# Optimization experiments

Hardware: AMD Instinct MI355X
Metric: run time of the kernel (lower is better)

Reference implementation:

```python
import jax, jax.numpy as jnp
import numpy as np

DIM = 4096
HIDDEN = 4096
B, N, M = 2, 512, 2048


def setup_inputs() -> dict:
    key = jax.random.key(0)
    k1, k2, k3, k4 = jax.random.split(key, 4)
    memory = jax.random.normal(k1, (B, M, DIM), dtype=jnp.bfloat16)
    inputs = jax.random.normal(k2, (B, N, DIM), dtype=jnp.bfloat16)
    # Linear(dim, hidden, bias=False): weight is [hidden, dim]; y = x @ W^T
    scale = 1.0 / np.sqrt(DIM)
    wq = (jax.random.normal(k3, (HIDDEN, DIM), dtype=jnp.float32) * scale).astype(jnp.bfloat16)
    wk = (jax.random.normal(k4, (HIDDEN, DIM), dtype=jnp.float32) * scale).astype(jnp.bfloat16)
    return {"memory": memory, "inputs": inputs, "wq": wq, "wk": wk, "seg_num": 100}


def reference(memory, inputs, wq, wk, seg_num):
    # xq = inputs @ Wq^T  [B, N, H];  mk = memory @ Wk^T  [B, M, H]
    xq = jnp.einsum('bnd,hd->bnh', inputs, wq)
    mk = jnp.einsum('bmd,hd->bmh', memory, wk)
    scores = jnp.einsum('bnh,bmh->bnm', xq, mk) / np.sqrt(HIDDEN)  # [B, N, M]
    scores = jax.nn.softmax(scores.astype(jnp.float32), axis=-1).astype(xq.dtype)
    # hist = seg_num - argmax over memory axis, flattened  [B*N]
    hist = (seg_num - jnp.argmax(scores, axis=2)).reshape(-1)
    browse = hist[0] < 4
    output = jnp.einsum('bnm,bmd->bnd', scores, memory)  # [B, N, dim]
    return output, hist, browse
```

## Files before the change

kernel.cpp:

```cpp
#include <hip/hip_runtime.h>

typedef unsigned short u16;
typedef unsigned int   u32;
typedef unsigned long long u64;
typedef __attribute__((ext_vector_type(8))) short bf16x8;
typedef __attribute__((ext_vector_type(8))) unsigned short u16x8;
typedef __attribute__((ext_vector_type(4))) float f32x4;

__device__ __forceinline__ float bf2f(u16 h){ u32 u = ((u32)h)<<16; return __builtin_bit_cast(float, u); }
__device__ __forceinline__ u16 f2bf(float f){
    u32 u = __builtin_bit_cast(u32, f);
    return (u16)((u + 0x7FFFu + ((u>>16)&1u)) >> 16);
}
__device__ __forceinline__ u16 ftrunc_bf(float f){
    return (u16)(__builtin_bit_cast(u32, f) >> 16);
}

__device__ __forceinline__ void gload16(const void* g, void* l){
    __builtin_amdgcn_global_load_lds((const __attribute__((address_space(1))) void*)g,
                                     (__attribute__((address_space(3))) void*)l, 16, 0, 0);
}


__global__ __launch_bounds__(256) void cvt_f2b(
    const float* __restrict__ in, u16* __restrict__ out, long n8)
{
    for (long i = (long)blockIdx.x * 256 + threadIdx.x; i < n8; i += (long)gridDim.x * 256){
        f32x4 a = *(const f32x4*)(in + i*8);
        f32x4 b = *(const f32x4*)(in + i*8 + 4);
        u16x8 o;
        #pragma unroll
        for (int j = 0; j < 4; j++){ o[j] = ftrunc_bf(a[j]); o[j+4] = ftrunc_bf(b[j]); }
        *(u16x8*)(out + i*8) = o;
    }
}

template<int OF32>
__device__ __forceinline__ void gemm_body(
    const u16* __restrict__ A, const u16* __restrict__ B, void* __restrict__ Cv,
    int K, int ldc, int rowA0, int rowB0, float scale,
    u16* lA, u16* lB)
{
    const int t = threadIdx.x, lane = t & 63, w = t >> 6;
    const int wr = w >> 1, wc = w & 1;

    f32x4 acc[4][4];
    #pragma unroll
    for (int i = 0; i < 4; i++)
        #pragma unroll
        for (int j = 0; j < 4; j++) acc[i][j] = (f32x4){0.f,0.f,0.f,0.f};

    const int r0 = t >> 2,         c0 = (t & 3) << 3;
    const int r1 = (t + 256) >> 2, c1 = ((t + 256) & 3) << 3;
    const int laneRow = lane & 15, laneK = (lane >> 4) << 3;

    const int nK = K >> 5;
    for (int kt = 0; kt < nK; ++kt){
        const int kk = kt << 5;
        gload16(A + (size_t)(rowA0 + r0) * K + kk + c0, &lA[t * 8]);
        gload16(B + (size_t)(rowB0 + r0) * K + kk + c0, &lB[t * 8]);
        gload16(A + (size_t)(rowA0 + r1) * K + kk + c1, &lA[(t + 256) * 8]);
        gload16(B + (size_t)(rowB0 + r1) * K + kk + c1, &lB[(t + 256) * 8]);
        __syncthreads();

        bf16x8 af[4], bfv[4];
        #pragma unroll
        for (int mi = 0; mi < 4; mi++)
            af[mi] = *(const bf16x8*)&lA[(wr*64 + mi*16 + laneRow) * 32 + laneK];
        #pragma unroll
        for (int ni = 0; ni < 4; ni++)
            bfv[ni] = *(const bf16x8*)&lB[(wc*64 + ni*16 + laneRow) * 32 + laneK];

        #pragma unroll
        for (int mi = 0; mi < 4; mi++)
            #pragma unroll
            for (int ni = 0; ni < 4; ni++)
                acc[mi][ni] = __builtin_amdgcn_mfma_f32_16x16x32_bf16(af[mi], bfv[ni], acc[mi][ni], 0, 0, 0);
        __syncthreads();
    }

    const int rowBase = rowA0 + wr*64;
    const int colBase = rowB0 + wc*64;
    #pragma unroll
    for (int mi = 0; mi < 4; mi++){
        #pragma unroll
        for (int ni = 0; ni < 4; ni++){
            f32x4 a = acc[mi][ni];
            const int cc = colBase + ni*16 + laneRow;
            const int rr = rowBase + mi*16 + ((lane >> 4) << 2);
            #pragma unroll
            for (int r = 0; r < 4; r++){
                const size_t idx = (size_t)(rr + r) * ldc + cc;
                float v = a[r] * scale;
                if (OF32) ((float*)Cv)[idx] = v;
                else      ((u16*)Cv)[idx]  = f2bf(v);
            }
        }
    }
}

template<int OF32>
__global__ __launch_bounds__(256) void gemm_b16(
    const u16* __restrict__ A, const u16* __restrict__ B, void* __restrict__ Cv,
    int K, int ldc, long aBatch, long bBatch, long cBatch, float scale)
{
    __shared__ u16 lA[128*32];
    __shared__ u16 lB[128*32];
    const int b = blockIdx.z;
    const u16* Ab = A + (size_t)b * aBatch;
    const u16* Bb = B + (size_t)b * bBatch;
    void* Cb = OF32 ? (void*)((float*)Cv + (size_t)b * cBatch)
                    : (void*)((u16*)Cv  + (size_t)b * cBatch);
    gemm_body<OF32>(Ab, Bb, Cb, K, ldc, blockIdx.y * 128, blockIdx.x * 128, scale, lA, lB);
}

__global__ __launch_bounds__(256) void proj_fused(
    const u16* __restrict__ mem16, const u16* __restrict__ wk16, u16* __restrict__ mk16,
    const u16* __restrict__ in16,  const u16* __restrict__ wq16, u16* __restrict__ xq16)
{
    __shared__ u16 lA[128*32];
    __shared__ u16 lB[128*32];
    const int z = blockIdx.z;
    const u16 *A, *B; u16* C;
    if (z < 2){
        A = mem16 + (size_t)z * 2048 * 4096; B = wk16; C = mk16 + (size_t)z * 2048 * 4096;
    } else {
        if (blockIdx.y >= 8) return;
        A = in16; B = wq16; C = xq16;
    }
    gemm_body<0>(A, B, C, 4096, 4096, blockIdx.y * 128, blockIdx.x * 128, 1.0f, lA, lB);
}

__global__ __launch_bounds__(256) void transpose_u16(
    const u16* __restrict__ in, u16* __restrict__ out)
{
    __shared__ u16 tile[64][65];
    const size_t bi = (size_t)blockIdx.z * 2048 * 4096;
    const size_t bo = (size_t)blockIdx.z * 4096 * 2048;
    const int c0 = blockIdx.x * 64;
    const int r0 = blockIdx.y * 64;
    const int x = threadIdx.x & 63, y = threadIdx.x >> 6;
    #pragma unroll
    for (int i = 0; i < 16; i++){
        int r = y + i*4;
        tile[r][x] = in[bi + (size_t)(r0 + r) * 4096 + c0 + x];
    }
    __syncthreads();
    #pragma unroll
    for (int i = 0; i < 16; i++){
        int c = y + i*4;
        out[bo + (size_t)(c0 + c) * 2048 + r0 + x] = tile[x][c];
    }
}

__device__ __forceinline__ u32 shfl_u32(u32 v, int srcx){ return (u32)__shfl_xor((int)v, srcx, 64); }
__device__ __forceinline__ u64 shflxor64(u64 x, int off){
    u32 lo = (u32)x, hi = (u32)(x >> 32);
    lo = shfl_u32(lo, off); hi = shfl_u32(hi, off);
    return (((u64)hi) << 32) | lo;
}

__global__ __launch_bounds__(256) void softmax_argmax16(
    const u16* __restrict__ sc16, u16* __restrict__ probs,
    float* __restrict__ dout, const int* __restrict__ segp)
{
    const int row = blockIdx.x;
    const u16* s = sc16 + (size_t)row * 2048;
    u16* p = probs + (size_t)row * 2048;
    const int t = threadIdx.x, lane = t & 63, w = t >> 6;

    u16x8 rv = *(const u16x8*)(s + (size_t)t * 8);
    float v[8];
    #pragma unroll
    for (int j = 0; j < 8; j++) v[j] = bf2f(rv[j]);

    float mx = v[0];
    #pragma unroll
    for (int j = 1; j < 8; j++) mx = fmaxf(mx, v[j]);
    #pragma unroll
    for (int off = 32; off; off >>= 1) mx = fmaxf(mx, __shfl_xor(mx, off, 64));
    __shared__ float smax[4];
    if (lane == 0) smax[w] = mx;
    __syncthreads();
    mx = fmaxf(fmaxf(smax[0], smax[1]), fmaxf(smax[2], smax[3]));

    float e[8]; float sum = 0.f;
    #pragma unroll
    for (int j = 0; j < 8; j++){ e[j] = expf(v[j] - mx); sum += e[j]; }
    #pragma unroll
    for (int off = 32; off; off >>= 1) sum += __shfl_xor(sum, off, 64);
    __shared__ float ssum[4];
    if (lane == 0) ssum[w] = sum;
    __syncthreads();
    sum = ssum[0] + ssum[1] + ssum[2] + ssum[3];

    u16x8 pv;
    u64 best = 0ull;
    #pragma unroll
    for (int j = 0; j < 8; j++){
        u16 pb = f2bf(e[j] / sum);
        pv[j] = pb;
        u64 key = (((u64)pb) << 32) | (u32)(0x7FFFFFFF - (t*8 + j));
        if (key > best) best = key;
    }
    *(u16x8*)(p + (size_t)t * 8) = pv;

    #pragma unroll
    for (int off = 32; off; off >>= 1){
        u64 o = shflxor64(best, off);
        if (o > best) best = o;
    }
    __shared__ u64 sb[4];
    if (lane == 0) sb[w] = best;
    __syncthreads();
    if (t == 0){
        u64 bb = sb[0];
        if (sb[1] > bb) bb = sb[1];
        if (sb[2] > bb) bb = sb[2];
        if (sb[3] > bb) bb = sb[3];
        int idx = 0x7FFFFFFF - (int)(bb & 0xFFFFFFFFu);
        float hv = (float)(segp[0] - idx);
        dout[4194304 + row] = hv;
        if (row == 0) dout[4195328] = (hv < 4.0f) ? 1.0f : 0.0f;
    }
}

template<int F32IN, int OF32>
__global__ __launch_bounds__(256) void gemm_bt(
    const void* __restrict__ Av, const void* __restrict__ Bv, void* __restrict__ Cv,
    int K, int ldc, float scale)
{
    __shared__ u16 lA[128*32];
    __shared__ u16 lB[128*32];
    const int rowA0 = blockIdx.y * 128;
    const int rowB0 = blockIdx.x * 128;
    const int t = threadIdx.x, lane = t & 63, w = t >> 6;
    const int wr = w >> 1, wc = w & 1;

    f32x4 acc[4][4];
    #pragma unroll
    for (int i = 0; i < 4; i++)
        #pragma unroll
        for (int j = 0; j < 4; j++) acc[i][j] = (f32x4){0.f,0.f,0.f,0.f};

    const int r0 = t >> 2,         c0 = (t & 3) << 3;
    const int r1 = (t + 256) >> 2, c1 = ((t + 256) & 3) << 3;
    const int laneRow = lane & 15, laneK = (lane >> 4) << 3;

    const int nK = K >> 5;
    for (int kt = 0; kt < nK; ++kt){
        const int kk = kt << 5;
        if (F32IN){
            const float* Af = (const float*)Av;
            const float* Bf = (const float*)Bv;
            f32x4 a00 = *(const f32x4*)&Af[(size_t)(rowA0 + r0) * K + kk + c0];
            f32x4 a01 = *(const f32x4*)&Af[(size_t)(rowA0 + r0) * K + kk + c0 + 4];
            f32x4 a10 = *(const f32x4*)&Af[(size_t)(rowA0 + r1) * K + kk + c1];
            f32x4 a11 = *(const f32x4*)&Af[(size_t)(rowA0 + r1) * K + kk + c1 + 4];
            f32x4 b00 = *(const f32x4*)&Bf[(size_t)(rowB0 + r0) * K + kk + c0];
            f32x4 b01 = *(const f32x4*)&Bf[(size_t)(rowB0 + r0) * K + kk + c0 + 4];
            f32x4 b10 = *(const f32x4*)&Bf[(size_t)(rowB0 + r1) * K + kk + c1];
            f32x4 b11 = *(const f32x4*)&Bf[(size_t)(rowB0 + r1) * K + kk + c1 + 4];
            u16x8 ua0, ua1, ub0, ub1;
            #pragma unroll
            for (int j = 0; j < 4; j++){
                ua0[j] = ftrunc_bf(a00[j]); ua0[j+4] = ftrunc_bf(a01[j]);
                ua1[j] = ftrunc_bf(a10[j]); ua1[j+4] = ftrunc_bf(a11[j]);
                ub0[j] = ftrunc_bf(b00[j]); ub0[j+4] = ftrunc_bf(b01[j]);
                ub1[j] = ftrunc_bf(b10[j]); ub1[j+4] = ftrunc_bf(b11[j]);
            }
            __syncthreads();
            *(u16x8*)&lA[(size_t)t * 8]         = ua0;
            *(u16x8*)&lA[(size_t)(t + 256) * 8] = ua1;
            *(u16x8*)&lB[(size_t)t * 8]         = ub0;
            *(u16x8*)&lB[(size_t)(t + 256) * 8] = ub1;
            __syncthreads();
        } else {
            const u16* Au = (const u16*)Av;
            const u16* Bu = (const u16*)Bv;
            gload16(Au + (size_t)(rowA0 + r0) * K + kk + c0, &lA[t * 8]);
            gload16(Bu + (size_t)(rowB0 + r0) * K + kk + c0, &lB[t * 8]);
            gload16(Au + (size_t)(rowA0 + r1) * K + kk + c1, &lA[(t + 256) * 8]);
            gload16(Bu + (size_t)(rowB0 + r1) * K + kk + c1, &lB[(t + 256) * 8]);
            __syncthreads();
        }

        bf16x8 af[4], bfv[4];
        #pragma unroll
        for (int mi = 0; mi < 4; mi++)
            af[mi] = *(const bf16x8*)&lA[(wr*64 + mi*16 + laneRow) * 32 + laneK];
        #pragma unroll
        for (int ni = 0; ni < 4; ni++)
            bfv[ni] = *(const bf16x8*)&lB[(wc*64 + ni*16 + laneRow) * 32 + laneK];

        #pragma unroll
        for (int mi = 0; mi < 4; mi++)
            #pragma unroll
            for (int ni = 0; ni < 4; ni++)
                acc[mi][ni] = __builtin_amdgcn_mfma_f32_16x16x32_bf16(af[mi], bfv[ni], acc[mi][ni], 0, 0, 0);
        if (!F32IN) __syncthreads();
    }

    const int rowBase = rowA0 + wr*64;
    const int colBase = rowB0 + wc*64;
    #pragma unroll
    for (int mi = 0; mi < 4; mi++){
        #pragma unroll
        for (int ni = 0; ni < 4; ni++){
            f32x4 a = acc[mi][ni];
            const int cc = colBase + ni*16 + laneRow;
            const int rr = rowBase + mi*16 + ((lane >> 4) << 2);
            #pragma unroll
            for (int r = 0; r < 4; r++){
                const size_t idx = (size_t)(rr + r) * ldc + cc;
                float v = a[r] * scale;
                if (OF32) ((float*)Cv)[idx] = v;
                else      ((u16*)Cv)[idx]  = f2bf(v);
            }
        }
    }
}

__global__ __launch_bounds__(256) void transpose_f2b(
    const float* __restrict__ in, u16* __restrict__ out)
{
    __shared__ u16 tile[64][65];
    const int c0 = blockIdx.x * 64;
    const int r0 = blockIdx.y * 64;
    const int x = threadIdx.x & 63, y = threadIdx.x >> 6;
    #pragma unroll
    for (int i = 0; i < 16; i++){
        int r = y + i*4;
        tile[r][x] = ftrunc_bf(in[(size_t)(r0 + r) * 4096 + c0 + x]);
    }
    __syncthreads();
    #pragma unroll
    for (int i = 0; i < 16; i++){
        int c = y + i*4;
        out[(size_t)(c0 + c) * 2048 + r0 + x] = tile[x][c];
    }
}

extern "C" void kernel_launch(void* const* d_in, const int* in_sizes, int n_in,
                              void* d_out, int out_size, void* d_ws, size_t ws_size,
                              hipStream_t stream)
{
    const float* memory = (const float*)d_in[0];
    const float* inputs = (const float*)d_in[1];
    const float* wq     = (const float*)d_in[2];
    const float* wk     = (const float*)d_in[3];
    const int*   seg    = (const int*)d_in[4];
    float* out = (float*)d_out;

    char* ws = (char*)d_ws;
    dim3 blk(256);

    if (ws_size >= (152ull << 20)){
        u16* mem16 = (u16*)(ws);
        u16* in16  = (u16*)(ws + 33554432);
        u16* wq16  = (u16*)(ws + 41943040);
        u16* wk16  = (u16*)(ws + 75497472);
        u16* xq16  = (u16*)(ws + 109051904);
        u16* mk16  = (u16*)(ws + 117440512);
        u16* sc16  = (u16*)(ws + 150994944);
        u16* pr    = (u16*)(ws + 155189248);
        u16* mt    = mk16;

        cvt_f2b<<<dim3(2048), blk, 0, stream>>>(memory, mem16, 2097152L);
        cvt_f2b<<<dim3(1024), blk, 0, stream>>>(inputs, in16,   524288L);
        cvt_f2b<<<dim3(2048), blk, 0, stream>>>(wq,     wq16,  2097152L);
        cvt_f2b<<<dim3(2048), blk, 0, stream>>>(wk,     wk16,  2097152L);

        proj_fused<<<dim3(32, 16, 3), blk, 0, stream>>>(mem16, wk16, mk16, in16, wq16, xq16);

        gemm_b16<0><<<dim3(16, 4, 2), blk, 0, stream>>>(xq16, mk16, sc16, 4096, 2048,
                                                        512L*4096, 2048L*4096, 512L*2048,
                                                        0.015625f);
        softmax_argmax16<<<dim3(1024), blk, 0, stream>>>(sc16, pr, out, seg);

        transpose_u16<<<dim3(64, 32, 2), blk, 0, stream>>>(mem16, mt);
        gemm_b16<1><<<dim3(32, 4, 2), blk, 0, stream>>>(pr, mt, out, 2048, 4096,
                                                        512L*2048, 4096L*2048, 512L*4096,
                                                        1.0f);
    } else {
        u16* xq16 = (u16*)(ws);
        u16* mk16 = (u16*)(ws + (8u<<20));
        u16* sc16 = (u16*)(ws + (24u<<20));
        u16* pr   = (u16*)(ws + (28u<<20));

        gemm_bt<1,0><<<dim3(32, 8, 1), blk, 0, stream>>>(inputs, wq, xq16, 4096, 4096, 1.0f);
        for (int b = 0; b < 2; ++b){
            const float* memb = memory + (size_t)b * 2048 * 4096;
            gemm_bt<1,0><<<dim3(32, 16, 1), blk, 0, stream>>>(memb, wk, mk16, 4096, 4096, 1.0f);
            gemm_bt<0,0><<<dim3(16, 4, 1), blk, 0, stream>>>(xq16 + (size_t)b*512*4096, mk16,
                                                             sc16 + (size_t)b*512*2048,
                                                             4096, 2048, 0.015625f);
        }
        softmax_argmax16<<<dim3(1024), blk, 0, stream>>>(sc16, pr, out, seg);
        for (int b = 0; b < 2; ++b){
            const float* memb = memory + (size_t)b * 2048 * 4096;
            transpose_f2b<<<dim3(64, 32, 1), blk, 0, stream>>>(memb, mk16);
            gemm_bt<0,1><<<dim3(32, 4, 1), blk, 0, stream>>>(pr + (size_t)b*512*2048, mk16,
                                                             out + (size_t)b*512*4096,
                                                             2048, 4096, 1.0f);
        }
    }
}
```

Baseline: 403.8 us.

## Compute memory key projection with a 256x256-tile double-buffered MFMA GEMM

Replaces the fused 128x128-tile projection with a new 512-thread kernel for the memory-key projection. It treats both batches as one 4096-row GEMM and uses 256x256 output tiles and 64-wide K tiles. Operands are double-buffered in 128KB of swizzled LDS via direct global-to-LDS loads, with raised wave priority around the MFMA loop. The goal is more data reuse per tile and better overlap of loads with compute. A sampled scalar check of the result is added, and if the check fails the old 128-tile kernel recomputes the projection. This adds serial verification work on every call, and the query projection now runs as its own GEMM launch.

```diff
diff --git a/kernel.cpp b/kernel.cpp
--- a/kernel.cpp
+++ b/kernel.cpp
@@ -21,17 +21,102 @@
                                      (__attribute__((address_space(3))) void*)l, 16, 0, 0);
 }
 
-
-__global__ __launch_bounds__(256) void cvt_f2b(
-    const float* __restrict__ in, u16* __restrict__ out, long n8)
-{
-    for (long i = (long)blockIdx.x * 256 + threadIdx.x; i < n8; i += (long)gridDim.x * 256){
-        f32x4 a = *(const f32x4*)(in + i*8);
-        f32x4 b = *(const f32x4*)(in + i*8 + 4);
-        u16x8 o;
-        #pragma unroll
-        for (int j = 0; j < 4; j++){ o[j] = ftrunc_bf(a[j]); o[j+4] = ftrunc_bf(b[j]); }
-        *(u16x8*)(out + i*8) = o;
+__device__ __forceinline__ int swz(int o){ return o ^ (((o >> 9) & 1) << 5); }
+
+__global__ __launch_bounds__(512, 2) void gemm8ph(
+    const u16* __restrict__ A, const u16* __restrict__ B, u16* __restrict__ C)
+{
+    extern __shared__ u16 lds[];
+    const int K = 4096, ldc = 4096;
+    const int t = threadIdx.x;
+    const int lane = t & 63, wid = t >> 6;
+    const int wr = wid >> 2, wc = wid & 3;
+    const int laneRow = lane & 15, laneK = (lane >> 4) << 3;
+    const int rowA0 = blockIdx.y * 256, rowB0 = blockIdx.x * 256;
+
+    f32x4 acc[8][4];
+    #pragma unroll
+    for (int i = 0; i < 8; i++)
+        #pragma unroll
+        for (int j = 0; j < 4; j++) acc[i][j] = (f32x4){0.f,0.f,0.f,0.f};
+
+    int sidx[4], srow[4], scg[4];
+    #pragma unroll
+    for (int i = 0; i < 4; i++){
+        int id = i * 512 + t;
+        sidx[i] = id;
+        srow[i] = id >> 3;
+        int cg  = id & 7;
+        scg[i]  = cg ^ (((id >> 5) & 1) << 1);
+    }
+
+    const int nT = K >> 6;
+    #pragma unroll
+    for (int i = 0; i < 4; i++){
+        gload16(A + (size_t)(rowA0 + srow[i]) * K + scg[i]*8, &lds[0*16384 + sidx[i]*8]);
+        gload16(B + (size_t)(rowB0 + srow[i]) * K + scg[i]*8, &lds[1*16384 + sidx[i]*8]);
+    }
+
+    for (int kt = 0; kt < nT; ++kt){
+        const int buf = kt & 1;
+        __builtin_amdgcn_s_barrier();
+        if (kt + 1 < nT){
+            const int kk = (kt + 1) << 6;
+            const int bo = (buf ^ 1) * 32768;
+            #pragma unroll
+            for (int i = 0; i < 4; i++){
+                gload16(A + (size_t)(rowA0 + srow[i]) * K + kk + scg[i]*8, &lds[bo + 0*16384 + sidx[i]*8]);
+                gload16(B + (size_t)(rowB0 + srow[i]) * K + kk + scg[i]*8, &lds[bo + 1*16384 + sidx[i]*8]);
+            }
+            asm volatile("s_waitcnt vmcnt(8)" ::: "memory");
+        } else {
+            asm volatile("s_waitcnt vmcnt(0)" ::: "memory");
+        }
+        __builtin_amdgcn_s_barrier();
+        __builtin_amdgcn_sched_barrier(0);
+
+        const char* lA = (const char*)&lds[(buf*2 + 0) * 16384];
+        const char* lB = (const char*)&lds[(buf*2 + 1) * 16384];
+
+        bf16x8 bfrag[2][4];
+        #pragma unroll
+        for (int kh = 0; kh < 2; kh++)
+            #pragma unroll
+            for (int ni = 0; ni < 4; ni++){
+                int raw = (wc*64 + ni*16 + laneRow)*128 + (kh*32 + laneK)*2;
+                bfrag[kh][ni] = *(const bf16x8*)(lB + swz(raw));
+            }
+
+        __builtin_amdgcn_s_setprio(1);
+        #pragma unroll
+        for (int mi = 0; mi < 8; mi++){
+            int raw0 = (wr*128 + mi*16 + laneRow)*128 + laneK*2;
+            int raw1 = raw0 + 64;
+            bf16x8 a0 = *(const bf16x8*)(lA + swz(raw0));
+            bf16x8 a1 = *(const bf16x8*)(lA + swz(raw1));
+            #pragma unroll
+            for (int ni = 0; ni < 4; ni++)
+                acc[mi][ni] = __builtin_amdgcn_mfma_f32_16x16x32_bf16(a0, bfrag[0][ni], acc[mi][ni], 0, 0, 0);
+            #pragma unroll
+            for (int ni = 0; ni < 4; ni++)
+                acc[mi][ni] = __builtin_amdgcn_mfma_f32_16x16x32_bf16(a1, bfrag[1][ni], acc[mi][ni], 0, 0, 0);
+        }
+        __builtin_amdgcn_s_setprio(0);
+    }
+
+    const int rowBase = rowA0 + wr*128;
+    const int colBase = rowB0 + wc*64;
+    #pragma unroll
+    for (int mi = 0; mi < 8; mi++){
+        #pragma unroll
+        for (int ni = 0; ni < 4; ni++){
+            f32x4 a = acc[mi][ni];
+            const int cc = colBase + ni*16 + laneRow;
+            const int rr = rowBase + mi*16 + ((lane >> 4) << 2);
+            #pragma unroll
+            for (int r = 0; r < 4; r++)
+                C[(size_t)(rr + r) * ldc + cc] = f2bf(a[r]);
+        }
     }
 }
 
@@ -114,21 +199,46 @@
     gemm_body<OF32>(Ab, Bb, Cb, K, ldc, blockIdx.y * 128, blockIdx.x * 128, scale, lA, lB);
 }
 
-__global__ __launch_bounds__(256) void proj_fused(
-    const u16* __restrict__ mem16, const u16* __restrict__ wk16, u16* __restrict__ mk16,
-    const u16* __restrict__ in16,  const u16* __restrict__ wq16, u16* __restrict__ xq16)
-{
+__global__ __launch_bounds__(256) void proj_redo(
+    const u32* __restrict__ flag,
+    const u16* __restrict__ mem16, const u16* __restrict__ wk16, u16* __restrict__ mk16)
+{
+    if (*flag == 0) return;
     __shared__ u16 lA[128*32];
     __shared__ u16 lB[128*32];
     const int z = blockIdx.z;
-    const u16 *A, *B; u16* C;
-    if (z < 2){
-        A = mem16 + (size_t)z * 2048 * 4096; B = wk16; C = mk16 + (size_t)z * 2048 * 4096;
-    } else {
-        if (blockIdx.y >= 8) return;
-        A = in16; B = wq16; C = xq16;
-    }
-    gemm_body<0>(A, B, C, 4096, 4096, blockIdx.y * 128, blockIdx.x * 128, 1.0f, lA, lB);
+    gemm_body<0>(mem16 + (size_t)z*2048*4096, wk16, mk16 + (size_t)z*2048*4096,
+                 4096, 4096, blockIdx.y * 128, blockIdx.x * 128, 1.0f, lA, lB);
+}
+
+__global__ void flag_init(u32* f){ if (threadIdx.x == 0) *f = 0; }
+
+__global__ __launch_bounds__(256) void vfy_mk(
+    const u16* __restrict__ mem16, const u16* __restrict__ wk16,
+    const u16* __restrict__ mk16, u32* __restrict__ flag)
+{
+    const int h = blockIdx.x * 256 + threadIdx.x;
+    const int tile = h >> 4, s = h & 15;
+    const int row = (tile >> 4) * 256 + ((s * 67) & 255);
+    const int col = (tile & 15) * 256 + ((s * 151 + 7) & 255);
+    const u16* a = mem16 + (size_t)row * 4096;
+    const u16* b = wk16 + (size_t)col * 4096;
+    float s0 = 0.f;
+    for (int k = 0; k < 4096; k++) s0 += bf2f(a[k]) * bf2f(b[k]);
+    if (fabsf(s0 - bf2f(mk16[(size_t)row * 4096 + col])) > 0.05f) atomicOr(flag, 1u);
+}
+
+__global__ __launch_bounds__(256) void cvt_f2b(
+    const float* __restrict__ in, u16* __restrict__ out, long n8)
+{
+    for (long i = (long)blockIdx.x * 256 + threadIdx.x; i < n8; i += (long)gridDim.x * 256){
+        f32x4 a = *(const f32x4*)(in + i*8);
+        f32x4 b = *(const f32x4*)(in + i*8 + 4);
+        u16x8 o;
+        #pragma unroll
+        for (int j = 0; j < 4; j++){ o[j] = ftrunc_bf(a[j]); o[j+4] = ftrunc_bf(b[j]); }
+        *(u16x8*)(out + i*8) = o;
+    }
 }
 
 __global__ __launch_bounds__(256) void transpose_u16(
@@ -365,14 +475,21 @@
         u16* sc16  = (u16*)(ws + 150994944);
         u16* pr    = (u16*)(ws + 155189248);
         u16* mt    = mk16;
+        u32* flag  = (u32*)sc16;
 
         cvt_f2b<<<dim3(2048), blk, 0, stream>>>(memory, mem16, 2097152L);
         cvt_f2b<<<dim3(1024), blk, 0, stream>>>(inputs, in16,   524288L);
         cvt_f2b<<<dim3(2048), blk, 0, stream>>>(wq,     wq16,  2097152L);
         cvt_f2b<<<dim3(2048), blk, 0, stream>>>(wk,     wk16,  2097152L);
 
-        proj_fused<<<dim3(32, 16, 3), blk, 0, stream>>>(mem16, wk16, mk16, in16, wq16, xq16);
-
+        gemm8ph<<<dim3(16, 16, 1), dim3(512), 131072, stream>>>(mem16, wk16, mk16);
+
+        flag_init<<<1, 64, 0, stream>>>(flag);
+        vfy_mk<<<dim3(16), blk, 0, stream>>>(mem16, wk16, mk16, flag);
+        proj_redo<<<dim3(32, 16, 2), blk, 0, stream>>>(flag, mem16, wk16, mk16);
+
+        gemm_b16<0><<<dim3(32, 8, 1), blk, 0, stream>>>(in16, wq16, xq16, 4096, 4096,
+                                                        0L, 0L, 0L, 1.0f);
         gemm_b16<0><<<dim3(16, 4, 2), blk, 0, stream>>>(xq16, mk16, sc16, 4096, 2048,
                                                         512L*4096, 2048L*4096, 512L*2048,
                                                         0.015625f);
```

New measurement: 563.9 us. +39.6%, slower.
